# Optimization experiments

Hardware: AMD Instinct MI355X
Metric: run time of the kernel (lower is better)

The kernel has to match this reference:

```python
import jax, jax.numpy as jnp
import numpy as np

B, T, C, H = 4, 2048, 1024, 16
D = C // H  # head_dim = 64


def setup_inputs() -> dict:
    key = jax.random.key(0)
    ks = jax.random.split(key, 5)
    s = 0.02
    return {
        "x": jax.random.normal(ks[0], (B, T, C), dtype=jnp.float32),
        "w_qkv": jax.random.normal(ks[1], (C, 3 * C), dtype=jnp.float32) * s,
        "b_qkv": jnp.zeros((3 * C,), dtype=jnp.float32),
        "w_proj": jax.random.normal(ks[2], (C, C), dtype=jnp.float32) * s,
        "b_proj": jnp.zeros((C,), dtype=jnp.float32),
    }


def reference(x, w_qkv, b_qkv, w_proj, b_proj):
    Bx, Tx, Cx = x.shape
    qkv = x @ w_qkv + b_qkv                      # [B,T,3C]
    q, k, v = jnp.split(qkv, 3, axis=-1)
    # [B,T,C] -> [B,H,T,D]
    q = q.reshape(Bx, Tx, H, D).transpose(0, 2, 1, 3)
    k = k.reshape(Bx, Tx, H, D).transpose(0, 2, 1, 3)
    v = v.reshape(Bx, Tx, H, D).transpose(0, 2, 1, 3)
    scale = 1.0 / np.sqrt(D).astype(np.float32)
    attn = jnp.einsum('bhqd,bhkd->bhqk', q, k) * scale   # [B,H,T,T]
    causal = jnp.tril(jnp.ones((Tx, Tx), dtype=bool))
    attn = jnp.where(causal[None, None], attn, -jnp.inf)
    attn = jax.nn.softmax(attn, axis=-1)
    out = jnp.einsum('bhqk,bhkd->bhqd', attn, v)          # [B,H,T,D]
    out = out.transpose(0, 2, 1, 3).reshape(Bx, Tx, Cx)   # [B,T,C]
    return out @ w_proj + b_proj
```

## Files before the change

kernel.cpp:

```cpp
#include <hip/hip_runtime.h>
#include <hip/hip_bf16.h>
#include <math.h>

using bf16 = __hip_bfloat16;
typedef __bf16 bf16x8 __attribute__((ext_vector_type(8)));
typedef float  f32x4  __attribute__((ext_vector_type(4)));
typedef unsigned short ushort8 __attribute__((ext_vector_type(8)));
typedef unsigned uint2v __attribute__((ext_vector_type(2)));

#define DEV __device__ __forceinline__

DEV void gld_lds16(const void* g, void* l) {
    __builtin_amdgcn_global_load_lds((const __attribute__((address_space(1))) void*)g,
                                     (__attribute__((address_space(3))) void*)l,
                                     16, 0, 0);
}

__global__ __launch_bounds__(256) void prep(const float* __restrict__ x,
                                            bf16* __restrict__ xb,
                                            const float* __restrict__ w_qkv,
                                            bf16* __restrict__ wqkvT,
                                            const float* __restrict__ w_proj,
                                            bf16* __restrict__ wprojT) {
    __shared__ float tile[32][33];
    int blk = blockIdx.x;
    int tid = threadIdx.x;
    if (blk < 8192) {
        int i = blk * 256 + tid;
        float4 f = ((const float4*)x)[i];
        __align__(8) bf16 o[4] = {__float2bfloat16(f.x), __float2bfloat16(f.y),
                                  __float2bfloat16(f.z), __float2bfloat16(f.w)};
        ((uint64_t*)xb)[i] = *(const uint64_t*)o;
        return;
    }
    const float* in;
    bf16* out;
    int R, Cn, bx, by;
    if (blk < 11264) {
        int bid = blk - 8192;
        in = w_qkv; out = wqkvT; R = 1024; Cn = 3072;
        bx = (bid % 96) * 32; by = (bid / 96) * 32;
    } else {
        int bid = blk - 11264;
        in = w_proj; out = wprojT; R = 1024; Cn = 1024;
        bx = (bid % 32) * 32; by = (bid / 32) * 32;
    }
    int tx = tid & 31, ty = tid >> 5;
    for (int i = ty; i < 32; i += 8)
        tile[i][tx] = in[(size_t)(by + i) * Cn + bx + tx];
    __syncthreads();
    for (int i = ty; i < 32; i += 8)
        out[(size_t)(bx + i) * R + by + tx] = __float2bfloat16(tile[tx][i]);
}

__global__ __launch_bounds__(256) void gemm_qkv(const bf16* __restrict__ A,
                                                const bf16* __restrict__ Bt,
                                                const float* __restrict__ bias,
                                                bf16* __restrict__ qb,
                                                bf16* __restrict__ kb,
                                                bf16* __restrict__ vTb) {
    constexpr int K = 1024, T = 2048;
    constexpr float CS = 0.18033688f;
    __shared__ __align__(16) bf16 Al[128 * 32];
    __shared__ __align__(16) bf16 Bl[128 * 32];
    __shared__ __align__(16) bf16 Et[32 * 136];
    int tid = threadIdx.x;
    int lane = tid & 63, w = tid >> 6;
    int wm = w >> 1, wn = w & 1;
    int l15 = lane & 15, quad = lane >> 4;
    int m0 = blockIdx.x * 128, n0 = blockIdx.y * 128;
    int l3 = l15 & 3;

    f32x4 acc[4][4] = {};
    for (int k0 = 0; k0 < K; k0 += 32) {
        __syncthreads();
        for (int it = 0; it < 2; ++it) {
            int e = (it * 256 + tid) * 8;
            int r = e >> 5, cu = (e >> 3) & 3;
            int cs = ((cu ^ (r & 3)) << 3);
            gld_lds16(A  + (size_t)(m0 + r) * K + k0 + cs, &Al[e]);
            gld_lds16(Bt + (size_t)(n0 + r) * K + k0 + cs, &Bl[e]);
        }
        __syncthreads();
        bf16x8 af[4], bfr[4];
        for (int i = 0; i < 4; ++i)
            af[i] = *(const bf16x8*)&Al[(wm * 64 + i * 16 + l15) * 32 + ((quad ^ l3) << 3)];
        for (int j = 0; j < 4; ++j)
            bfr[j] = *(const bf16x8*)&Bl[(wn * 64 + j * 16 + l15) * 32 + ((quad ^ l3) << 3)];
        for (int i = 0; i < 4; ++i)
            for (int j = 0; j < 4; ++j)
                acc[i][j] = __builtin_amdgcn_mfma_f32_16x16x32_bf16(af[i], bfr[j], acc[i][j], 0, 0, 0);
    }

    int mode = (blockIdx.y < 8) ? 0 : (blockIdx.y < 16 ? 1 : 2);
    float bv[4];
    for (int j = 0; j < 4; ++j)
        bv[j] = bias[n0 + wn * 64 + j * 16 + l15];
    float scl = (mode == 0) ? CS : 1.0f;

    for (int i = 0; i < 4; ++i) {
        __syncthreads();
        for (int j = 0; j < 4; ++j)
            for (int v = 0; v < 4; ++v)
                Et[(wm * 16 + quad * 4 + v) * 136 + wn * 64 + j * 16 + l15] =
                    __float2bfloat16((acc[i][j][v] + bv[j]) * scl);
        __syncthreads();
        if (mode < 2) {
            int r = tid >> 3, cc = (tid & 7) * 16;
            int m = m0 + i * 16 + (r < 16 ? r : r + 48);
            int b = m >> 11, t = m & 2047;
            int n = (n0 & 1023) + cc;
            int h = n >> 6, d = n & 63;
            bf16* dst = (mode == 0 ? qb : kb) + (((size_t)(b * 16 + h)) * T + t) * 64 + d;
            ushort8 u0 = *(const ushort8*)&Et[r * 136 + cc];
            ushort8 u1 = *(const ushort8*)&Et[r * 136 + cc + 8];
            *(ushort8*)dst = u0;
            *(ushort8*)(dst + 8) = u1;
        } else {
            int run = tid >> 7, d = tid & 127;
            int t0 = m0 + i * 16 + run * 64;
            int b = t0 >> 11, tt = t0 & 2047;
            int n = (n0 & 1023) + d;
            int h = n >> 6, dd = n & 63;
            __align__(16) bf16 tmp[16];
            for (int jj = 0; jj < 16; ++jj)
                tmp[jj] = Et[(run * 16 + jj) * 136 + d];
            bf16* dst = vTb + (((size_t)(b * 16 + h)) * 64 + dd) * T + tt;
            *(ushort8*)dst = *(const ushort8*)tmp;
            *(ushort8*)(dst + 8) = *(const ushort8*)(tmp + 8);
        }
    }
}

__global__ __launch_bounds__(256, 4) void flash_attn(const bf16* __restrict__ qb,
                                                     const bf16* __restrict__ kbuf,
                                                     const bf16* __restrict__ vT,
                                                     bf16* __restrict__ ob) {
    constexpr int T = 2048;
    __shared__ __align__(16) bf16 Kl[2][64 * 64];
    __shared__ __align__(16) bf16 Vl[64 * 64];
    __shared__ __align__(16) bf16 Pl[128 * 64];
    int tid = threadIdx.x;
    int lane = tid & 63, w = tid >> 6;
    int l15 = lane & 15, quad = lane >> 4;

    int g = blockIdx.x;
    int quarter = g >> 8;
    int j = (g >> 6) & 3;
    int bh = g & 63;
    int xq;
    switch (quarter) {
        case 0:  xq = 15 - j; break;
        case 1:  xq = 8 + j;  break;
        case 2:  xq = 4 + j;  break;
        default: xq = 3 - j;  break;
    }
    int q0 = xq << 7;
    const bf16* qbase = qb   + (size_t)bh * T * 64;
    const bf16* kbase = kbuf + (size_t)bh * T * 64;
    const bf16* vbase = vT   + (size_t)bh * 64 * T;

    int qg[2];
    bf16x8 qa[2][2];
#pragma unroll
    for (int s = 0; s < 2; ++s) {
        qg[s] = q0 + w * 32 + s * 16 + l15;
#pragma unroll
        for (int c = 0; c < 2; ++c)
            qa[s][c] = *(const bf16x8*)(qbase + (size_t)qg[s] * 64 + c * 32 + quad * 8);
    }

    bf16x8 ones;
#pragma unroll
    for (int i = 0; i < 8; ++i) ones[i] = (__bf16)1.0f;

    f32x4 O[2][4] = {};
    f32x4 O1[2] = {};
    int h7 = l15 & 7;

    int off0 = tid * 8, off1 = (256 + tid) * 8;
    int r0 = off0 >> 6, cb0 = (off0 >> 3) & 7;
    int r1 = off1 >> 6, cb1 = (off1 >> 3) & 7;
    int kc0 = (cb0 ^ (r0 & 7)) << 3, kc1 = (cb1 ^ (r1 & 7)) << 3;

    int prow0 = w * 32 + l15;
    int nit = 2 * xq + 2;

    bf16x8 vr0 = *(const bf16x8*)(vbase + (size_t)r0 * T + kc0);
    bf16x8 vr1 = *(const bf16x8*)(vbase + (size_t)r1 * T + kc1);
    gld_lds16(kbase + (size_t)r0 * 64 + kc0, &Kl[0][off0]);
    gld_lds16(kbase + (size_t)r1 * 64 + kc1, &Kl[0][off1]);
    *(bf16x8*)&Vl[off0] = vr0;
    *(bf16x8*)&Vl[off1] = vr1;

    for (int t = 0; t < nit; ++t) {
        int cur = t & 1;
        __syncthreads();
        bool pre = (t + 1 < nit);
        if (pre) {
            int kb2 = (t + 1) << 6, nxt = cur ^ 1;
            vr0 = *(const bf16x8*)(vbase + (size_t)r0 * T + kb2 + kc0);
            vr1 = *(const bf16x8*)(vbase + (size_t)r1 * T + kb2 + kc1);
            gld_lds16(kbase + (size_t)(kb2 + r0) * 64 + kc0, &Kl[nxt][off0]);
            gld_lds16(kbase + (size_t)(kb2 + r1) * 64 + kc1, &Kl[nxt][off1]);
        }
        int kb = t << 6;
        bool maskt = (t >= nit - 2);

#pragma unroll
        for (int jn = 0; jn < 4; ++jn) {
            int row = jn * 16 + l15;
            bf16x8 a0 = *(const bf16x8*)&Kl[cur][row * 64 + ((quad ^ h7) << 3)];
            bf16x8 a1 = *(const bf16x8*)&Kl[cur][row * 64 + (((4 + quad) ^ h7) << 3)];
            f32x4 sa[2] = {};
            __builtin_amdgcn_s_setprio(1);
            sa[0] = __builtin_amdgcn_mfma_f32_16x16x32_bf16(a0, qa[0][0], sa[0], 0, 0, 0);
            sa[0] = __builtin_amdgcn_mfma_f32_16x16x32_bf16(a1, qa[0][1], sa[0], 0, 0, 0);
            sa[1] = __builtin_amdgcn_mfma_f32_16x16x32_bf16(a0, qa[1][0], sa[1], 0, 0, 0);
            sa[1] = __builtin_amdgcn_mfma_f32_16x16x32_bf16(a1, qa[1][1], sa[1], 0, 0, 0);
            __builtin_amdgcn_s_setprio(0);
            int ubase = jn * 2 + (quad >> 1);
            int lowo = (quad & 1) << 2;
#pragma unroll
            for (int s = 0; s < 2; ++s) {
                float p[4];
#pragma unroll
                for (int v = 0; v < 4; ++v) {
                    float e = __builtin_amdgcn_exp2f(sa[s][v]);
                    if (maskt) {
                        int key = kb + jn * 16 + quad * 4 + v;
                        e = (key <= qg[s]) ? e : 0.f;
                    }
                    p[v] = e;
                }
                unsigned lo, hi;
                asm("v_cvt_pk_bf16_f32 %0, %1, %2" : "=v"(lo) : "v"(p[0]), "v"(p[1]));
                asm("v_cvt_pk_bf16_f32 %0, %1, %2" : "=v"(hi) : "v"(p[2]), "v"(p[3]));
                uint2v pv;
                pv[0] = lo;
                pv[1] = hi;
                int prow = prow0 + s * 16;
                *(uint2v*)&Pl[prow * 64 + ((ubase ^ h7) << 3) + lowo] = pv;
            }
        }
        asm volatile("s_waitcnt lgkmcnt(0)" ::: "memory");
        bf16x8 pf[2][2];
#pragma unroll
        for (int s = 0; s < 2; ++s) {
            int prow = prow0 + s * 16;
#pragma unroll
            for (int c = 0; c < 2; ++c)
                pf[s][c] = *(const bf16x8*)&Pl[prow * 64 + (((c * 4 + quad) ^ h7) << 3)];
        }

        __builtin_amdgcn_s_setprio(1);
#pragma unroll
        for (int s = 0; s < 2; ++s) {
            O1[s] = __builtin_amdgcn_mfma_f32_16x16x32_bf16(pf[s][0], ones, O1[s], 0, 0, 0);
            O1[s] = __builtin_amdgcn_mfma_f32_16x16x32_bf16(pf[s][1], ones, O1[s], 0, 0, 0);
        }
        __builtin_amdgcn_s_setprio(0);

#pragma unroll
        for (int jd = 0; jd < 4; ++jd) {
            int vrow = jd * 16 + l15;
            bf16x8 v0 = *(const bf16x8*)&Vl[vrow * 64 + ((quad ^ h7) << 3)];
            bf16x8 v1 = *(const bf16x8*)&Vl[vrow * 64 + (((4 + quad) ^ h7) << 3)];
            __builtin_amdgcn_s_setprio(1);
            O[0][jd] = __builtin_amdgcn_mfma_f32_16x16x32_bf16(pf[0][0], v0, O[0][jd], 0, 0, 0);
            O[0][jd] = __builtin_amdgcn_mfma_f32_16x16x32_bf16(pf[0][1], v1, O[0][jd], 0, 0, 0);
            O[1][jd] = __builtin_amdgcn_mfma_f32_16x16x32_bf16(pf[1][0], v0, O[1][jd], 0, 0, 0);
            O[1][jd] = __builtin_amdgcn_mfma_f32_16x16x32_bf16(pf[1][1], v1, O[1][jd], 0, 0, 0);
            __builtin_amdgcn_s_setprio(0);
        }

        __builtin_amdgcn_s_barrier();
        if (pre) {
            *(bf16x8*)&Vl[off0] = vr0;
            *(bf16x8*)&Vl[off1] = vr1;
        }
    }

    int b = bh >> 4, h = bh & 15;
#pragma unroll
    for (int s = 0; s < 2; ++s) {
        float linv[4];
#pragma unroll
        for (int v = 0; v < 4; ++v) linv[v] = 1.f / O1[s][v];
#pragma unroll
        for (int jd = 0; jd < 4; ++jd) {
#pragma unroll
            for (int v = 0; v < 4; ++v) {
                int qr = q0 + w * 32 + s * 16 + quad * 4 + v;
                ob[((size_t)(b * T + qr)) * 1024 + h * 64 + jd * 16 + l15] =
                    __float2bfloat16(O[s][jd][v] * linv[v]);
            }
        }
    }
}

__global__ __launch_bounds__(256) void gemm_proj(const bf16* __restrict__ A,
                                                 const bf16* __restrict__ Bt,
                                                 const float* __restrict__ bias,
                                                 float* __restrict__ out) {
    constexpr int K = 1024, N = 1024;
    __shared__ __align__(16) bf16 Al[128 * 32];
    __shared__ __align__(16) bf16 Bl[128 * 32];
    int tid = threadIdx.x;
    int lane = tid & 63, w = tid >> 6;
    int wm = w >> 1, wn = w & 1;
    int l15 = lane & 15, quad = lane >> 4;
    int m0 = blockIdx.x * 128, n0 = blockIdx.y * 128;
    int l3 = l15 & 3;

    f32x4 acc[4][4] = {};
    for (int k0 = 0; k0 < K; k0 += 32) {
        __syncthreads();
        for (int it = 0; it < 2; ++it) {
            int e = (it * 256 + tid) * 8;
            int r = e >> 5, cu = (e >> 3) & 3;
            int cs = ((cu ^ (r & 3)) << 3);
            gld_lds16(A  + (size_t)(m0 + r) * K + k0 + cs, &Al[e]);
            gld_lds16(Bt + (size_t)(n0 + r) * K + k0 + cs, &Bl[e]);
        }
        __syncthreads();
        bf16x8 af[4], bfr[4];
        for (int i = 0; i < 4; ++i)
            af[i] = *(const bf16x8*)&Al[(wm * 64 + i * 16 + l15) * 32 + ((quad ^ l3) << 3)];
        for (int j = 0; j < 4; ++j)
            bfr[j] = *(const bf16x8*)&Bl[(wn * 64 + j * 16 + l15) * 32 + ((quad ^ l3) << 3)];
        for (int i = 0; i < 4; ++i)
            for (int j = 0; j < 4; ++j)
                acc[i][j] = __builtin_amdgcn_mfma_f32_16x16x32_bf16(af[i], bfr[j], acc[i][j], 0, 0, 0);
    }
    for (int i = 0; i < 4; ++i) {
        int mbase = m0 + wm * 64 + i * 16 + quad * 4;
        for (int j = 0; j < 4; ++j) {
            int n = n0 + wn * 64 + j * 16 + l15;
            float bv = bias[n];
            for (int v = 0; v < 4; ++v)
                out[(size_t)(mbase + v) * N + n] = acc[i][j][v] + bv;
        }
    }
}

extern "C" void kernel_launch(void* const* d_in, const int* in_sizes, int n_in,
                              void* d_out, int out_size, void* d_ws, size_t ws_size,
                              hipStream_t stream) {
    (void)in_sizes; (void)n_in; (void)out_size; (void)ws_size;
    const float* x      = (const float*)d_in[0];
    const float* w_qkv  = (const float*)d_in[1];
    const float* b_qkv  = (const float*)d_in[2];
    const float* w_proj = (const float*)d_in[3];
    const float* b_proj = (const float*)d_in[4];
    float* out = (float*)d_out;

    char* ws = (char*)d_ws;
    bf16* xb     = (bf16*)(ws);
    bf16* wqkvT  = (bf16*)(ws + (16u << 20));
    bf16* wprojT = (bf16*)(ws + (22u << 20));
    bf16* qbuf   = (bf16*)(ws + (24u << 20));
    bf16* kbuf   = (bf16*)(ws + (40u << 20));
    bf16* vTb    = (bf16*)(ws + (72u << 20));
    bf16* ob     = (bf16*)(ws + (56u << 20));

    prep<<<12288, 256, 0, stream>>>(x, xb, w_qkv, wqkvT, w_proj, wprojT);
    gemm_qkv<<<dim3(64, 24), 256, 0, stream>>>(xb, wqkvT, b_qkv, qbuf, kbuf, vTb);
    flash_attn<<<1024, 256, 0, stream>>>(qbuf, kbuf, vTb, ob);
    gemm_proj<<<dim3(64, 8), 256, 0, stream>>>(ob, wprojT, b_proj, out);
}
```

Baseline: 241.3 us.

## Replace LDS round-trip for P fragments with permlane swaps in registers

```diff
diff --git a/kernel.cpp b/kernel.cpp
--- a/kernel.cpp
+++ b/kernel.cpp
@@ -6,7 +6,7 @@
 typedef __bf16 bf16x8 __attribute__((ext_vector_type(8)));
 typedef float  f32x4  __attribute__((ext_vector_type(4)));
 typedef unsigned short ushort8 __attribute__((ext_vector_type(8)));
-typedef unsigned uint2v __attribute__((ext_vector_type(2)));
+typedef unsigned uint4v __attribute__((ext_vector_type(4)));
 
 #define DEV __device__ __forceinline__
 
@@ -139,7 +139,6 @@
     constexpr int T = 2048;
     __shared__ __align__(16) bf16 Kl[2][64 * 64];
     __shared__ __align__(16) bf16 Vl[64 * 64];
-    __shared__ __align__(16) bf16 Pl[128 * 64];
     int tid = threadIdx.x;
     int lane = tid & 63, w = tid >> 6;
     int l15 = lane & 15, quad = lane >> 4;
@@ -183,7 +182,6 @@
     int r1 = off1 >> 6, cb1 = (off1 >> 3) & 7;
     int kc0 = (cb0 ^ (r0 & 7)) << 3, kc1 = (cb1 ^ (r1 & 7)) << 3;
 
-    int prow0 = w * 32 + l15;
     int nit = 2 * xq + 2;
 
     bf16x8 vr0 = *(const bf16x8*)(vbase + (size_t)r0 * T + kc0);
@@ -207,6 +205,7 @@
         int kb = t << 6;
         bool maskt = (t >= nit - 2);
 
+        unsigned Dq[2][4][2];
 #pragma unroll
         for (int jn = 0; jn < 4; ++jn) {
             int row = jn * 16 + l15;
@@ -219,8 +218,6 @@
             sa[1] = __builtin_amdgcn_mfma_f32_16x16x32_bf16(a0, qa[1][0], sa[1], 0, 0, 0);
             sa[1] = __builtin_amdgcn_mfma_f32_16x16x32_bf16(a1, qa[1][1], sa[1], 0, 0, 0);
             __builtin_amdgcn_s_setprio(0);
-            int ubase = jn * 2 + (quad >> 1);
-            int lowo = (quad & 1) << 2;
 #pragma unroll
             for (int s = 0; s < 2; ++s) {
                 float p[4];
@@ -236,22 +233,28 @@
                 unsigned lo, hi;
                 asm("v_cvt_pk_bf16_f32 %0, %1, %2" : "=v"(lo) : "v"(p[0]), "v"(p[1]));
                 asm("v_cvt_pk_bf16_f32 %0, %1, %2" : "=v"(hi) : "v"(p[2]), "v"(p[3]));
-                uint2v pv;
-                pv[0] = lo;
-                pv[1] = hi;
-                int prow = prow0 + s * 16;
-                *(uint2v*)&Pl[prow * 64 + ((ubase ^ h7) << 3) + lowo] = pv;
+                Dq[s][jn][0] = lo;
+                Dq[s][jn][1] = hi;
             }
         }
-        asm volatile("s_waitcnt lgkmcnt(0)" ::: "memory");
+
         bf16x8 pf[2][2];
 #pragma unroll
-        for (int s = 0; s < 2; ++s) {
-            int prow = prow0 + s * 16;
-#pragma unroll
-            for (int c = 0; c < 2; ++c)
-                pf[s][c] = *(const bf16x8*)&Pl[prow * 64 + (((c * 4 + quad) ^ h7) << 3)];
-        }
+        for (int s = 0; s < 2; ++s)
+#pragma unroll
+            for (int c = 0; c < 2; ++c) {
+                uint4v wv;
+#pragma unroll
+                for (int h = 0; h < 2; ++h) {
+                    unsigned X = Dq[s][2 * c][h];
+                    unsigned Y = Dq[s][2 * c + 1][h];
+                    asm("v_permlane32_swap_b32 %0, %1" : "+v"(X), "+v"(Y));
+                    asm("v_permlane16_swap_b32 %0, %1" : "+v"(X), "+v"(Y));
+                    wv[h]     = X;
+                    wv[2 + h] = Y;
+                }
+                pf[s][c] = __builtin_bit_cast(bf16x8, wv);
+            }
 
         __builtin_amdgcn_s_setprio(1);
 #pragma unroll
```

After: 238.8 us, median of 2. Within noise of the previous version (-1.1%).
